# Performance work log

Measured on AMD Instinct MI355X. Metric: run time of the kernel, lower is better.

Reference implementation:

```python
import jax, jax.numpy as jnp
import numpy as np

GRID = (128, 128, 16)
VSIZE = 0.5  # voxel_size, pc_range = 0
B, V, N, K, C = 2, 100000, 8192, 8, 64
EPS = 1e-5
OFFSETS = [(dx, dy, dz) for dx in (-1, 0, 1) for dy in (-1, 0, 1) for dz in (-1, 0, 1)]


def setup_inputs() -> dict:
    key = jax.random.key(0)
    ks = jax.random.split(key, 8)
    world = jnp.array([GRID[0] * VSIZE, GRID[1] * VSIZE, GRID[2] * VSIZE], jnp.float32)
    keypoints = jax.random.uniform(ks[0], (B, N, K, 3), jnp.float32) * world
    query_feature = jax.random.normal(ks[1], (B, N, C), jnp.float32)
    voxel_feature = jax.random.normal(ks[2], (B, V, C), jnp.float32)
    # unique voxel coords per batch (hash-map / sparse-tensor semantics)
    cells = GRID[0] * GRID[1] * GRID[2]
    perm = jax.vmap(lambda k: jax.random.permutation(k, cells)[:V])(jax.random.split(ks[3], B))
    x = perm // (GRID[1] * GRID[2])
    rem = perm % (GRID[1] * GRID[2])
    voxel_coords = jnp.stack([x, rem // GRID[2], rem % GRID[2]], -1).astype(jnp.int32)
    W1 = jax.random.normal(ks[4], (27, C, C), jnp.float32) * 0.05
    W2 = jax.random.normal(ks[5], (27, C, C), jnp.float32) * 0.05
    proj_W = jax.random.normal(ks[6], (C, C), jnp.float32) / np.sqrt(C).astype(np.float32)
    proj_b = jnp.zeros((C,), jnp.float32)
    return dict(keypoints=keypoints, query_feature=query_feature,
                voxel_feature=voxel_feature, voxel_coords=voxel_coords,
                W1=W1, bn1_gamma=jnp.ones((C,), jnp.float32), bn1_beta=jnp.zeros((C,), jnp.float32),
                W2=W2, bn2_gamma=jnp.ones((C,), jnp.float32), bn2_beta=jnp.zeros((C,), jnp.float32),
                proj_W=proj_W, proj_b=proj_b)


def _subm_conv(feats, grid, cb, cxyz, W):
    # feats: (M, C); grid: (B, X, Y, Z) int32 flat row index or -1; W: (27, Cin, Cout)
    out = jnp.zeros((feats.shape[0], W.shape[-1]), feats.dtype)
    for k, (dx, dy, dz) in enumerate(OFFSETS):
        nx, ny, nz = cxyz[:, 0] + dx, cxyz[:, 1] + dy, cxyz[:, 2] + dz
        valid = (nx >= 0) & (nx < GRID[0]) & (ny >= 0) & (ny < GRID[1]) & (nz >= 0) & (nz < GRID[2])
        nidx = grid[cb, jnp.clip(nx, 0, GRID[0] - 1), jnp.clip(ny, 0, GRID[1] - 1), jnp.clip(nz, 0, GRID[2] - 1)]
        nidx = jnp.where(valid, nidx, -1)
        nf = jnp.where((nidx >= 0)[:, None], feats[jnp.maximum(nidx, 0)], jnp.zeros((), feats.dtype))
        out = out + nf @ W[k]
    return out


def _bn_relu(x, gamma, beta):
    # BatchNorm1d in training mode: batch stats (biased var), then ReLU
    mu = x.mean(0)
    var = jnp.var(x, axis=0)
    return jax.nn.relu((x - mu) * jax.lax.rsqrt(var + EPS) * gamma + beta)


def reference(keypoints, query_feature, voxel_feature, voxel_coords,
              W1, bn1_gamma, bn1_beta, W2, bn2_gamma, bn2_beta, proj_W, proj_b):
    coords = voxel_coords.reshape(-1, 3).astype(jnp.int32)
    cb = jnp.repeat(jnp.arange(B, dtype=jnp.int32), V)
    # dense grid hash: cell -> flat voxel row, -1 if empty (replaces Python dict)
    grid = jnp.full((B,) + GRID, -1, jnp.int32)
    grid = grid.at[cb, coords[:, 0], coords[:, 1], coords[:, 2]].set(jnp.arange(B * V, dtype=jnp.int32))
    feats = voxel_feature.reshape(-1, C)
    feats = _bn_relu(_subm_conv(feats, grid, cb, coords, W1), bn1_gamma, bn1_beta)
    feats = _bn_relu(_subm_conv(feats, grid, cb, coords, W2), bn2_gamma, bn2_beta)
    # quantize keypoints (pc_range = 0, trunc == floor since coords >= 0)
    q = (keypoints / VSIZE).astype(jnp.int32)
    q = jnp.clip(q, 0, jnp.array(GRID, jnp.int32) - 1)  # (B, N, K, 3)
    bidx = jnp.arange(B, dtype=jnp.int32)[:, None, None]
    idx = grid[bidx, q[..., 0], q[..., 1], q[..., 2]]   # (B, N, K); -1 -> fallback row 0
    sampled = feats[jnp.maximum(idx, 0)]                 # (B, N, K, C)
    fused = (sampled.mean(2) + query_feature) @ proj_W.T + proj_b
    voxel_indices = jnp.concatenate(
        [jnp.broadcast_to(bidx[..., None], (B, N, K, 1)), q], axis=-1).reshape(-1, 4)
    return fused, voxel_indices
```

## Files before the change

kernel.cpp:

```cpp
#include <hip/hip_runtime.h>
#include <hip/hip_bf16.h>
#include <math.h>

#define GX 128
#define GY 128
#define GZ 16
#define CELLS (GX*GY*GZ)
#define NCELLT (NB*CELLS)
#define NB 2
#define NV 100000
#define NM (NB*NV)
#define NN 8192
#define NK 8
#define NC 64
#define EPSV 1e-5f
#define TM 128
#define NTILE 196
#define NBLK (8*NTILE)

typedef __attribute__((ext_vector_type(8))) short short8;
typedef __attribute__((ext_vector_type(4))) float floatx4;

__device__ __forceinline__ float bf2f(unsigned short u) {
    unsigned int x = ((unsigned int)u) << 16;
    return __builtin_bit_cast(float, x);
}
__device__ __forceinline__ unsigned short f2bf(float f) {
    unsigned int u = __builtin_bit_cast(unsigned int, f);
    return (unsigned short)((u + 0x7fffu + ((u >> 16) & 1u)) >> 16);
}

__global__ void k_init(int* __restrict__ grid, float* __restrict__ stats,
                       unsigned short* __restrict__ featA) {
    int i = blockIdx.x * 256 + threadIdx.x;
    if (i < NCELLT) grid[i] = -1;
    else if (i < NCELLT + 512) stats[i - NCELLT] = 0.f;
    else if (i < NCELLT + 512 + 64) featA[(size_t)NM * 64 + (i - NCELLT - 512)] = 0;
}

__global__ void k_scatter(const int* __restrict__ coords, int* __restrict__ grid) {
    int gid = blockIdx.x * 256 + threadIdx.x;
    if (gid >= NM) return;
    int b = (gid >= NV) ? 1 : 0;
    int x = coords[gid * 3 + 0];
    int y = coords[gid * 3 + 1];
    int z = coords[gid * 3 + 2];
    grid[((b * GX + x) * GY + y) * GZ + z] = gid;
}

__global__ void k_count(const int* __restrict__ grid, int* __restrict__ bcnt) {
    __shared__ int wt[4];
    int t = threadIdx.x;
    int occ = (grid[blockIdx.x * 256 + t] >= 0) ? 1 : 0;
    int w = t >> 6;
    unsigned long long m = __ballot(occ);
    if ((t & 63) == 0) wt[w] = __popcll(m);
    __syncthreads();
    if (t == 0) bcnt[blockIdx.x] = wt[0] + wt[1] + wt[2] + wt[3];
}

__global__ void k_scan2048(const int* __restrict__ bcnt, int* __restrict__ boff) {
    __shared__ int s[256];
    int t = threadIdx.x;
    int v[8], sum = 0;
    #pragma unroll
    for (int j = 0; j < 8; ++j) {
        int x = bcnt[t * 8 + j];
        v[j] = sum;
        sum += x;
    }
    s[t] = sum;
    __syncthreads();
    for (int off = 1; off < 256; off <<= 1) {
        int x = (t >= off) ? s[t - off] : 0;
        __syncthreads();
        s[t] += x;
        __syncthreads();
    }
    int excl = s[t] - sum;
    #pragma unroll
    for (int j = 0; j < 8; ++j) boff[t * 8 + j] = excl + v[j];
}

__global__ void k_assign(const int* __restrict__ gold, const int* __restrict__ boff,
                         int* __restrict__ gnew, int* __restrict__ perm,
                         int* __restrict__ scell) {
    __shared__ int wt[4];
    int t = threadIdx.x;
    int cell = blockIdx.x * 256 + t;
    int old = gold[cell];
    int occ = (old >= 0) ? 1 : 0;
    int w = t >> 6, lane = t & 63;
    unsigned long long m = __ballot(occ);
    int lp = __popcll(m & ((1ULL << lane) - 1ULL));
    if (lane == 63) wt[w] = lp + occ;
    __syncthreads();
    int wbase = 0;
    #pragma unroll
    for (int j = 0; j < 4; ++j) if (j < w) wbase += wt[j];
    int nid = boff[blockIdx.x] + wbase + lp;
    if (occ) {
        gnew[cell] = nid;
        perm[nid] = old;
        scell[nid] = cell;
    } else {
        gnew[cell] = -1;
    }
}

__global__ void k_fb(const int* __restrict__ vcoords, const int* __restrict__ gnew,
                     int* __restrict__ fbp) {
    if (threadIdx.x == 0 && blockIdx.x == 0) {
        int cell = (vcoords[0] * GY + vcoords[1]) * GZ + vcoords[2];
        fbp[0] = gnew[cell];
    }
}

__global__ void k_wprep(const float* __restrict__ W1, const float* __restrict__ W2,
                        unsigned short* __restrict__ Wt1, unsigned short* __restrict__ Wt2) {
    int e = blockIdx.x * 256 + threadIdx.x;
    if (e >= 27 * 512) return;
    int lane = e & 63;
    int fr = (e >> 6) & 7;
    int k = e >> 9;
    int ct = fr >> 1, ks = fr & 1;
    int quad = lane >> 4, n16 = lane & 15;
    int co = ct * 16 + n16;
    #pragma unroll
    for (int j = 0; j < 8; ++j) {
        int ci = ks * 32 + quad * 8 + j;
        Wt1[(size_t)e * 8 + j] = f2bf(W1[(k << 12) + ci * 64 + co]);
        Wt2[(size_t)e * 8 + j] = f2bf(W2[(k << 12) + ci * 64 + co]);
    }
}

__global__ void k_tobf16s(const float* __restrict__ in, const int* __restrict__ perm,
                          unsigned short* __restrict__ out) {
    int i = blockIdx.x * 256 + threadIdx.x;
    if (i >= NM * 8) return;
    int mrow = i >> 3, part = i & 7;
    int src = perm[mrow];
    const float4* s = (const float4*)(in + (size_t)src * 64 + part * 8);
    float4 a = s[0], b = s[1];
    ushort4 lo, hi;
    lo.x = f2bf(a.x); lo.y = f2bf(a.y); lo.z = f2bf(a.z); lo.w = f2bf(a.w);
    hi.x = f2bf(b.x); hi.y = f2bf(b.y); hi.z = f2bf(b.z); hi.w = f2bf(b.w);
    ushort4* d = (ushort4*)(out + (size_t)mrow * 64 + part * 8);
    d[0] = lo; d[1] = hi;
}

__global__ __launch_bounds__(256, 4) void k_conv(
    const unsigned short* __restrict__ feats, const int* __restrict__ scell,
    const int* __restrict__ grid, const unsigned short* __restrict__ Wt,
    unsigned short* __restrict__ out, float* __restrict__ gsum, float* __restrict__ gsq)
{
    __shared__ int s_nidx[27 * TM];
    __shared__ int s_c[TM];

    int tid = threadIdx.x;
    int bid = blockIdx.x;
    int tile = (bid & 7) * NTILE + (bid >> 3);
    int m0 = tile * TM;

    if (tid < TM) {
        int m = m0 + tid;
        s_c[tid] = (m < NM) ? scell[m] : -1;
    }
    __syncthreads();

    for (int e = tid; e < 27 * TM; e += 256) {
        int k = e >> 7;
        int r = e & (TM - 1);
        int dx = k / 9 - 1, dy = (k / 3) % 3 - 1, dz = k % 3 - 1;
        int cell = s_c[r];
        int ni = -1;
        if (cell >= 0) {
            int x = (cell >> 11) & 127, y = (cell >> 4) & 127, z = cell & 15;
            int nx = x + dx, ny = y + dy, nz = z + dz;
            if (nx >= 0 && nx < GX && ny >= 0 && ny < GY && nz >= 0 && nz < GZ)
                ni = grid[cell + dx * (GY * GZ) + dy * GZ + dz];
        }
        s_nidx[k * TM + r] = ni;
    }
    __syncthreads();

    int w = tid >> 6, lane = tid & 63;
    int quad = lane >> 4, n16 = lane & 15;
    const int* nrow = s_nidx + w * 32 + n16;
    const unsigned short* fq = feats + quad * 8;

    short8 afr[2][4];
    short8 bfr[8];

    auto issueA = [&](int k, short8* af) {
        int ni0 = nrow[k * TM];
        int ni1 = nrow[k * TM + 16];
        ni0 = (ni0 < 0) ? NM : ni0;
        ni1 = (ni1 < 0) ? NM : ni1;
        const unsigned short* r0 = fq + (size_t)ni0 * 64;
        const unsigned short* r1 = fq + (size_t)ni1 * 64;
        af[0] = *(const short8*)(r0);
        af[1] = *(const short8*)(r0 + 32);
        af[2] = *(const short8*)(r1);
        af[3] = *(const short8*)(r1 + 32);
    };
    auto issueB = [&](int k, short8* bf) {
        const unsigned short* wb = Wt + ((size_t)k * 512 + lane) * 8;
        #pragma unroll
        for (int fr = 0; fr < 8; ++fr)
            bf[fr] = *(const short8*)(wb + fr * 512);
    };

    floatx4 acc[2][4];
    #pragma unroll
    for (int rt = 0; rt < 2; ++rt)
        #pragma unroll
        for (int ct = 0; ct < 4; ++ct)
            acc[rt][ct] = (floatx4){0.f, 0.f, 0.f, 0.f};

    issueA(0, afr[0]);
    __builtin_amdgcn_sched_barrier(0);

    #pragma unroll
    for (int k = 0; k < 27; ++k) {
        issueB(k, bfr);
        if (k + 1 < 27) issueA(k + 1, afr[(k + 1) & 1]);
        __builtin_amdgcn_sched_barrier(0);

        const short8* ac = afr[k & 1];
        #pragma unroll
        for (int ks = 0; ks < 2; ++ks)
            #pragma unroll
            for (int rt = 0; rt < 2; ++rt)
                #pragma unroll
                for (int ct = 0; ct < 4; ++ct)
                    acc[rt][ct] = __builtin_amdgcn_mfma_f32_16x16x32_bf16(
                        ac[rt * 2 + ks], bfr[ct * 2 + ks], acc[rt][ct], 0, 0, 0);
        __builtin_amdgcn_sched_barrier(0);
    }

    #pragma unroll
    for (int rt = 0; rt < 2; ++rt) {
        int rbase = m0 + w * 32 + rt * 16 + quad * 4;
        #pragma unroll
        for (int rg = 0; rg < 4; ++rg) {
            int m = rbase + rg;
            if (m < NM) {
                #pragma unroll
                for (int ct = 0; ct < 4; ++ct)
                    out[(size_t)m * 64 + ct * 16 + n16] = f2bf(acc[rt][ct][rg]);
            }
        }
    }

    float ps[4], pq[4];
    #pragma unroll
    for (int ct = 0; ct < 4; ++ct) { ps[ct] = 0.f; pq[ct] = 0.f; }
    #pragma unroll
    for (int rt = 0; rt < 2; ++rt)
        #pragma unroll
        for (int ct = 0; ct < 4; ++ct)
            #pragma unroll
            for (int rg = 0; rg < 4; ++rg) {
                float v = acc[rt][ct][rg];
                ps[ct] += v;
                pq[ct] += v * v;
            }
    #pragma unroll
    for (int ct = 0; ct < 4; ++ct) {
        ps[ct] += __shfl_xor(ps[ct], 16);
        ps[ct] += __shfl_xor(ps[ct], 32);
        pq[ct] += __shfl_xor(pq[ct], 16);
        pq[ct] += __shfl_xor(pq[ct], 32);
    }
    __syncthreads();
    float* red = (float*)s_nidx;
    if (lane < 16) {
        #pragma unroll
        for (int ct = 0; ct < 4; ++ct) {
            red[w * 64 + ct * 16 + n16]       = ps[ct];
            red[256 + w * 64 + ct * 16 + n16] = pq[ct];
        }
    }
    __syncthreads();
    if (tid < 64) {
        float ts = 0.f, tq = 0.f;
        #pragma unroll
        for (int ww = 0; ww < 4; ++ww) {
            ts += red[ww * 64 + tid];
            tq += red[256 + ww * 64 + tid];
        }
        atomicAdd(gsum + tid, ts);
        atomicAdd(gsq + tid, tq);
    }
}

__global__ void k_bncoef(const float* __restrict__ gsum, const float* __restrict__ gsq,
                         const float* __restrict__ gamma, const float* __restrict__ beta,
                         float* __restrict__ coef) {
    int c = threadIdx.x;
    if (c >= 64) return;
    float mu = gsum[c] / (float)NM;
    float var = gsq[c] / (float)NM - mu * mu;
    float scale = gamma[c] / sqrtf(var + EPSV);
    coef[c] = scale;
    coef[64 + c] = beta[c] - mu * scale;
}

__global__ void k_bnapply(const unsigned short* __restrict__ in, const float* __restrict__ coef,
                          unsigned short* __restrict__ out) {
    int i = blockIdx.x * 256 + threadIdx.x;
    if (i >= NM * 8) return;
    int c8 = (i & 7) * 8;
    uint4 v = ((const uint4*)in)[i];
    unsigned int vv[4] = {v.x, v.y, v.z, v.w};
    unsigned int oo[4];
    #pragma unroll
    for (int j = 0; j < 4; ++j) {
        int c = c8 + j * 2;
        float lo = bf2f((unsigned short)(vv[j] & 0xffffu));
        float hi = bf2f((unsigned short)(vv[j] >> 16));
        lo = fmaxf(lo * coef[c]     + coef[64 + c],     0.f);
        hi = fmaxf(hi * coef[c + 1] + coef[64 + c + 1], 0.f);
        oo[j] = (unsigned int)f2bf(lo) | ((unsigned int)f2bf(hi) << 16);
    }
    uint4 o = {oo[0], oo[1], oo[2], oo[3]};
    ((uint4*)out)[i] = o;
}

__global__ __launch_bounds__(256) void k_sample(
    const float* __restrict__ kp, const float* __restrict__ query,
    const unsigned short* __restrict__ conv2, const float* __restrict__ coef2,
    const int* __restrict__ grid, const int* __restrict__ fbp,
    const float* __restrict__ projW, const float* __restrict__ projB,
    float* __restrict__ out_fused, float* __restrict__ out_vi)
{
    __shared__ float s_pw[64 * 65];
    __shared__ float s_mean[4][64];
    __shared__ int   s_idx[4][8];

    int tid = threadIdx.x;
    for (int e = tid; e < 4096; e += 256) {
        int co = e >> 6, c = e & 63;
        s_pw[co * 65 + c] = projW[e];
    }

    int w = tid >> 6, lane = tid & 63;
    int row = blockIdx.x * 4 + w;
    int b = row >> 13;
    float sc = coef2[lane];
    float sh = coef2[64 + lane];
    int fb = fbp[0];
    __syncthreads();

    if (lane < 8) {
        int kk = lane;
        const float* kpp = kp + ((size_t)row * 8 + kk) * 3;
        int qx = min(max((int)(kpp[0] * 2.0f), 0), GX - 1);
        int qy = min(max((int)(kpp[1] * 2.0f), 0), GY - 1);
        int qz = min(max((int)(kpp[2] * 2.0f), 0), GZ - 1);
        s_idx[w][kk] = grid[((b * GX + qx) * GY + qy) * GZ + qz];
        float4 vi = make_float4((float)b, (float)qx, (float)qy, (float)qz);
        *(float4*)(out_vi + ((size_t)row * 8 + kk) * 4) = vi;
    }
    __syncthreads();

    float acc = 0.f;
    #pragma unroll
    for (int kk = 0; kk < 8; ++kk) {
        int gi = s_idx[w][kk];
        gi = gi < 0 ? fb : gi;
        float v = bf2f(conv2[(size_t)gi * 64 + lane]);
        acc += fmaxf(v * sc + sh, 0.f);
    }
    float mean = acc * 0.125f + query[(size_t)row * 64 + lane];
    s_mean[w][lane] = mean;
    __syncthreads();

    float f = projB[lane];
    const float* pwr = s_pw + lane * 65;
    const float* mv = s_mean[w];
    #pragma unroll 8
    for (int c = 0; c < 64; ++c) f += mv[c] * pwr[c];
    out_fused[(size_t)row * 64 + lane] = f;
}

extern "C" void kernel_launch(void* const* d_in, const int* in_sizes, int n_in,
                              void* d_out, int out_size, void* d_ws, size_t ws_size,
                              hipStream_t stream) {
    const float* keypoints = (const float*)d_in[0];
    const float* query     = (const float*)d_in[1];
    const float* vfeat     = (const float*)d_in[2];
    const int*   vcoords   = (const int*)d_in[3];
    const float* W1        = (const float*)d_in[4];
    const float* g1        = (const float*)d_in[5];
    const float* b1        = (const float*)d_in[6];
    const float* W2        = (const float*)d_in[7];
    const float* g2        = (const float*)d_in[8];
    const float* b2        = (const float*)d_in[9];
    const float* pW        = (const float*)d_in[10];
    const float* pb        = (const float*)d_in[11];

    char* ws = (char*)d_ws;
    int*            gold  = (int*)ws;
    int*            gnew  = (int*)(ws + 2097152);
    float*          stats = (float*)(ws + 4194304);
    int*            fbp   = (int*)(ws + 4196352);
    int*            bcnt  = (int*)(ws + 4196608);
    int*            boff  = (int*)(ws + 4204800);
    int*            perm  = (int*)(ws + 4212992);
    int*            scell = (int*)(ws + 5012992);
    unsigned short* Wt1   = (unsigned short*)(ws + 5812992);
    unsigned short* Wt2   = (unsigned short*)(ws + 6034176);
    unsigned short* featA = (unsigned short*)(ws + 6255360);
    unsigned short* convo = (unsigned short*)(ws + 31855488);

    float* sum1 = stats,       *sq1 = stats + 64,  *coef1 = stats + 128;
    float* sum2 = stats + 256, *sq2 = stats + 320, *coef2 = stats + 384;

    int initN = NCELLT + 512 + 64;
    k_init<<<(initN + 255) / 256, 256, 0, stream>>>(gold, stats, featA);
    k_scatter<<<(NM + 255) / 256, 256, 0, stream>>>(vcoords, gold);

    k_count<<<NCELLT / 256, 256, 0, stream>>>(gold, bcnt);
    k_scan2048<<<1, 256, 0, stream>>>(bcnt, boff);
    k_assign<<<NCELLT / 256, 256, 0, stream>>>(gold, boff, gnew, perm, scell);
    k_fb<<<1, 64, 0, stream>>>(vcoords, gnew, fbp);

    k_wprep<<<(27 * 512 + 255) / 256, 256, 0, stream>>>(W1, W2, Wt1, Wt2);
    k_tobf16s<<<(NM * 8 + 255) / 256, 256, 0, stream>>>(vfeat, perm, featA);

    k_conv<<<NBLK, 256, 0, stream>>>(featA, scell, gnew, Wt1, convo, sum1, sq1);
    k_bncoef<<<1, 64, 0, stream>>>(sum1, sq1, g1, b1, coef1);
    k_bnapply<<<(NM * 8 + 255) / 256, 256, 0, stream>>>(convo, coef1, featA);

    k_conv<<<NBLK, 256, 0, stream>>>(featA, scell, gnew, Wt2, convo, sum2, sq2);
    k_bncoef<<<1, 64, 0, stream>>>(sum2, sq2, g2, b2, coef2);

    float* out_fused = (float*)d_out;
    float* out_vi = out_fused + (size_t)NB * NN * NC;
    k_sample<<<(NB * NN) / 4, 256, 0, stream>>>(keypoints, query, convo, coef2, gnew, fbp,
                                                pW, pb, out_fused, out_vi);
}
```

Before: 378.5 us.

## Stage conv weight slices through double-buffered LDS instead of per-wave global loads

Each block now loads the 27 weight slices cooperatively into a double-buffered shared-memory array, with register staging for the next slice, instead of having each of the four waves load the full slice from global/L2. This cuts redundant weight traffic by four times per block. In exchange it adds a __syncthreads per offset and 16 KB of LDS, which may lower occupancy and serialize the waves.

```diff
diff --git a/kernel.cpp b/kernel.cpp
--- a/kernel.cpp
+++ b/kernel.cpp
@@ -156,6 +156,7 @@
 {
     __shared__ int s_nidx[27 * TM];
     __shared__ int s_c[TM];
+    __shared__ unsigned short s_bw[2][4096];
 
     int tid = threadIdx.x;
     int bid = blockIdx.x;
@@ -190,8 +191,18 @@
     const unsigned short* fq = feats + quad * 8;
 
     short8 afr[2][4];
-    short8 bfr[8];
-
+    uint4 sreg[2];
+
+    auto stageLoad = [&](int k) {
+        const uint4* src = (const uint4*)(Wt + (size_t)k * 4096) + tid;
+        sreg[0] = src[0];
+        sreg[1] = src[256];
+    };
+    auto stageStore = [&](int k) {
+        uint4* dst = (uint4*)s_bw[k & 1] + tid;
+        dst[0]   = sreg[0];
+        dst[256] = sreg[1];
+    };
     auto issueA = [&](int k, short8* af) {
         int ni0 = nrow[k * TM];
         int ni1 = nrow[k * TM + 16];
@@ -204,12 +215,6 @@
         af[2] = *(const short8*)(r1);
         af[3] = *(const short8*)(r1 + 32);
     };
-    auto issueB = [&](int k, short8* bf) {
-        const unsigned short* wb = Wt + ((size_t)k * 512 + lane) * 8;
-        #pragma unroll
-        for (int fr = 0; fr < 8; ++fr)
-            bf[fr] = *(const short8*)(wb + fr * 512);
-    };
 
     floatx4 acc[2][4];
     #pragma unroll
@@ -218,25 +223,37 @@
         for (int ct = 0; ct < 4; ++ct)
             acc[rt][ct] = (floatx4){0.f, 0.f, 0.f, 0.f};
 
+    stageLoad(0);
     issueA(0, afr[0]);
-    __builtin_amdgcn_sched_barrier(0);
+    stageStore(0);
+    __syncthreads();
 
     #pragma unroll
     for (int k = 0; k < 27; ++k) {
-        issueB(k, bfr);
-        if (k + 1 < 27) issueA(k + 1, afr[(k + 1) & 1]);
+        if (k + 1 < 27) {
+            stageLoad(k + 1);
+            issueA(k + 1, afr[(k + 1) & 1]);
+        }
         __builtin_amdgcn_sched_barrier(0);
 
-        const short8* ac = afr[k & 1];
-        #pragma unroll
-        for (int ks = 0; ks < 2; ++ks)
+        const unsigned short* bb = s_bw[k & 1];
+        #pragma unroll
+        for (int ks = 0; ks < 2; ++ks) {
+            short8 bfr[4];
+            #pragma unroll
+            for (int ct = 0; ct < 4; ++ct)
+                bfr[ct] = *(const short8*)(bb + (ct * 2 + ks) * 512 + lane * 8);
             #pragma unroll
             for (int rt = 0; rt < 2; ++rt)
                 #pragma unroll
                 for (int ct = 0; ct < 4; ++ct)
                     acc[rt][ct] = __builtin_amdgcn_mfma_f32_16x16x32_bf16(
-                        ac[rt * 2 + ks], bfr[ct * 2 + ks], acc[rt][ct], 0, 0, 0);
+                        afr[k & 1][rt * 2 + ks], bfr[ct], acc[rt][ct], 0, 0, 0);
+        }
         __builtin_amdgcn_sched_barrier(0);
+
+        if (k + 1 < 27) stageStore(k + 1);
+        __syncthreads();
     }
 
     #pragma unroll
```

Measured after the change: 439.7 us. +16.2%, slower.

## Double conv tile rows and stage weights in LDS in phases

Applied to the files above, without the earlier changes.

The sparse conv kernel now processes 256 rows per block (64 per wave) instead of 128. Weights for 7 kernel offsets at a time are staged in shared memory rather than loaded from global memory per wave. Neighbor indices are also computed per phase, and the weights are padded to 28 offsets with zeros so the four phases divide evenly. This is meant to cut redundant weight traffic and amortize it over more MFMAs, at the cost of higher register and LDS use (occupancy bound lowered to 2), a wasted zero offset, and extra barriers per phase.

```diff
diff --git a/kernel.cpp b/kernel.cpp
--- a/kernel.cpp
+++ b/kernel.cpp
@@ -14,9 +14,10 @@
 #define NK 8
 #define NC 64
 #define EPSV 1e-5f
-#define TM 128
-#define NTILE 196
+#define TM 256
+#define NTILE 98
 #define NBLK (8*NTILE)
+#define KPH 7
 
 typedef __attribute__((ext_vector_type(8))) short short8;
 typedef __attribute__((ext_vector_type(4))) float floatx4;
@@ -119,7 +120,7 @@
 __global__ void k_wprep(const float* __restrict__ W1, const float* __restrict__ W2,
                         unsigned short* __restrict__ Wt1, unsigned short* __restrict__ Wt2) {
     int e = blockIdx.x * 256 + threadIdx.x;
-    if (e >= 27 * 512) return;
+    if (e >= 28 * 512) return;
     int lane = e & 63;
     int fr = (e >> 6) & 7;
     int k = e >> 9;
@@ -129,8 +130,13 @@
     #pragma unroll
     for (int j = 0; j < 8; ++j) {
         int ci = ks * 32 + quad * 8 + j;
-        Wt1[(size_t)e * 8 + j] = f2bf(W1[(k << 12) + ci * 64 + co]);
-        Wt2[(size_t)e * 8 + j] = f2bf(W2[(k << 12) + ci * 64 + co]);
+        unsigned short w1 = 0, w2 = 0;
+        if (k < 27) {
+            w1 = f2bf(W1[(k << 12) + ci * 64 + co]);
+            w2 = f2bf(W2[(k << 12) + ci * 64 + co]);
+        }
+        Wt1[(size_t)e * 8 + j] = w1;
+        Wt2[(size_t)e * 8 + j] = w2;
     }
 }
 
@@ -149,12 +155,13 @@
     d[0] = lo; d[1] = hi;
 }
 
-__global__ __launch_bounds__(256, 4) void k_conv(
+__global__ __launch_bounds__(256, 2) void k_conv(
     const unsigned short* __restrict__ feats, const int* __restrict__ scell,
     const int* __restrict__ grid, const unsigned short* __restrict__ Wt,
     unsigned short* __restrict__ out, float* __restrict__ gsum, float* __restrict__ gsq)
 {
-    __shared__ int s_nidx[27 * TM];
+    __shared__ unsigned short s_b[KPH * 4096];
+    __shared__ int s_nidx[KPH * TM];
     __shared__ int s_c[TM];
 
     int tid = threadIdx.x;
@@ -162,86 +169,94 @@
     int tile = (bid & 7) * NTILE + (bid >> 3);
     int m0 = tile * TM;
 
-    if (tid < TM) {
+    {
         int m = m0 + tid;
         s_c[tid] = (m < NM) ? scell[m] : -1;
     }
-    __syncthreads();
-
-    for (int e = tid; e < 27 * TM; e += 256) {
-        int k = e >> 7;
-        int r = e & (TM - 1);
-        int dx = k / 9 - 1, dy = (k / 3) % 3 - 1, dz = k % 3 - 1;
-        int cell = s_c[r];
-        int ni = -1;
-        if (cell >= 0) {
-            int x = (cell >> 11) & 127, y = (cell >> 4) & 127, z = cell & 15;
-            int nx = x + dx, ny = y + dy, nz = z + dz;
-            if (nx >= 0 && nx < GX && ny >= 0 && ny < GY && nz >= 0 && nz < GZ)
-                ni = grid[cell + dx * (GY * GZ) + dy * GZ + dz];
-        }
-        s_nidx[k * TM + r] = ni;
-    }
-    __syncthreads();
 
     int w = tid >> 6, lane = tid & 63;
     int quad = lane >> 4, n16 = lane & 15;
-    const int* nrow = s_nidx + w * 32 + n16;
     const unsigned short* fq = feats + quad * 8;
 
-    short8 afr[2][4];
-    short8 bfr[8];
-
-    auto issueA = [&](int k, short8* af) {
-        int ni0 = nrow[k * TM];
-        int ni1 = nrow[k * TM + 16];
-        ni0 = (ni0 < 0) ? NM : ni0;
-        ni1 = (ni1 < 0) ? NM : ni1;
-        const unsigned short* r0 = fq + (size_t)ni0 * 64;
-        const unsigned short* r1 = fq + (size_t)ni1 * 64;
-        af[0] = *(const short8*)(r0);
-        af[1] = *(const short8*)(r0 + 32);
-        af[2] = *(const short8*)(r1);
-        af[3] = *(const short8*)(r1 + 32);
+    short8 afr[2][8];
+
+    auto issueA = [&](int kk, short8* af) {
+        #pragma unroll
+        for (int rt = 0; rt < 4; ++rt) {
+            int ni = s_nidx[kk * TM + w * 64 + rt * 16 + n16];
+            ni = (ni < 0) ? NM : ni;
+            const unsigned short* r0 = fq + (size_t)ni * 64;
+            af[rt * 2 + 0] = *(const short8*)(r0);
+            af[rt * 2 + 1] = *(const short8*)(r0 + 32);
+        }
     };
-    auto issueB = [&](int k, short8* bf) {
-        const unsigned short* wb = Wt + ((size_t)k * 512 + lane) * 8;
-        #pragma unroll
-        for (int fr = 0; fr < 8; ++fr)
-            bf[fr] = *(const short8*)(wb + fr * 512);
-    };
-
-    floatx4 acc[2][4];
-    #pragma unroll
-    for (int rt = 0; rt < 2; ++rt)
+
+    floatx4 acc[4][4];
+    #pragma unroll
+    for (int rt = 0; rt < 4; ++rt)
         #pragma unroll
         for (int ct = 0; ct < 4; ++ct)
             acc[rt][ct] = (floatx4){0.f, 0.f, 0.f, 0.f};
 
-    issueA(0, afr[0]);
-    __builtin_amdgcn_sched_barrier(0);
-
-    #pragma unroll
-    for (int k = 0; k < 27; ++k) {
-        issueB(k, bfr);
-        if (k + 1 < 27) issueA(k + 1, afr[(k + 1) & 1]);
+    const uint4* wt4 = (const uint4*)Wt;
+
+    for (int ph = 0; ph < 4; ++ph) {
+        int k0 = ph * KPH;
+        __syncthreads();
+        #pragma unroll
+        for (int i = 0; i < KPH * 2; ++i)
+            ((uint4*)s_b)[i * 256 + tid] = wt4[(size_t)k0 * 512 + i * 256 + tid];
+        #pragma unroll
+        for (int j = 0; j < KPH; ++j) {
+            int e = j * 256 + tid;
+            int kk = e >> 8;
+            int r = e & 255;
+            int k = k0 + kk;
+            int ni = -1;
+            if (k < 27) {
+                int dx = k / 9 - 1, dy = (k / 3) % 3 - 1, dz = k % 3 - 1;
+                int cell = s_c[r];
+                if (cell >= 0) {
+                    int x = (cell >> 11) & 127, y = (cell >> 4) & 127, z = cell & 15;
+                    int nx = x + dx, ny = y + dy, nz = z + dz;
+                    if (nx >= 0 && nx < GX && ny >= 0 && ny < GY && nz >= 0 && nz < GZ)
+                        ni = grid[cell + dx * (GY * GZ) + dy * GZ + dz];
+                }
+            }
+            s_nidx[kk * TM + r] = ni;
+        }
+        __syncthreads();
+
+        issueA(0, afr[0]);
         __builtin_amdgcn_sched_barrier(0);
 
-        const short8* ac = afr[k & 1];
-        #pragma unroll
-        for (int ks = 0; ks < 2; ++ks)
+        #pragma unroll
+        for (int kk = 0; kk < KPH; ++kk) {
+            if (kk + 1 < KPH) issueA(kk + 1, afr[(kk + 1) & 1]);
+            __builtin_amdgcn_sched_barrier(0);
+
+            const unsigned short* bb = s_b + kk * 4096;
+            short8 bfr[8];
             #pragma unroll
-            for (int rt = 0; rt < 2; ++rt)
+            for (int fr = 0; fr < 8; ++fr)
+                bfr[fr] = *(const short8*)(bb + fr * 512 + lane * 8);
+
+            const short8* ac = afr[kk & 1];
+            #pragma unroll
+            for (int ks = 0; ks < 2; ++ks)
                 #pragma unroll
-                for (int ct = 0; ct < 4; ++ct)
-                    acc[rt][ct] = __builtin_amdgcn_mfma_f32_16x16x32_bf16(
-                        ac[rt * 2 + ks], bfr[ct * 2 + ks], acc[rt][ct], 0, 0, 0);
-        __builtin_amdgcn_sched_barrier(0);
-    }
-
-    #pragma unroll
-    for (int rt = 0; rt < 2; ++rt) {
-        int rbase = m0 + w * 32 + rt * 16 + quad * 4;
+                for (int rt = 0; rt < 4; ++rt)
+                    #pragma unroll
+                    for (int ct = 0; ct < 4; ++ct)
+                        acc[rt][ct] = __builtin_amdgcn_mfma_f32_16x16x32_bf16(
+                            ac[rt * 2 + ks], bfr[ct * 2 + ks], acc[rt][ct], 0, 0, 0);
+            __builtin_amdgcn_sched_barrier(0);
+        }
+    }
+
+    #pragma unroll
+    for (int rt = 0; rt < 4; ++rt) {
+        int rbase = m0 + w * 64 + rt * 16 + quad * 4;
         #pragma unroll
         for (int rg = 0; rg < 4; ++rg) {
             int m = rbase + rg;
@@ -257,7 +272,7 @@
     #pragma unroll
     for (int ct = 0; ct < 4; ++ct) { ps[ct] = 0.f; pq[ct] = 0.f; }
     #pragma unroll
-    for (int rt = 0; rt < 2; ++rt)
+    for (int rt = 0; rt < 4; ++rt)
         #pragma unroll
         for (int ct = 0; ct < 4; ++ct)
             #pragma unroll
@@ -411,9 +426,9 @@
     int*            perm  = (int*)(ws + 4212992);
     int*            scell = (int*)(ws + 5012992);
     unsigned short* Wt1   = (unsigned short*)(ws + 5812992);
-    unsigned short* Wt2   = (unsigned short*)(ws + 6034176);
-    unsigned short* featA = (unsigned short*)(ws + 6255360);
-    unsigned short* convo = (unsigned short*)(ws + 31855488);
+    unsigned short* Wt2   = (unsigned short*)(ws + 6042368);
+    unsigned short* featA = (unsigned short*)(ws + 6271744);
+    unsigned short* convo = (unsigned short*)(ws + 31871872);
 
     float* sum1 = stats,       *sq1 = stats + 64,  *coef1 = stats + 128;
     float* sum2 = stats + 256, *sq2 = stats + 320, *coef2 = stats + 384;
@@ -427,7 +442,7 @@
     k_assign<<<NCELLT / 256, 256, 0, stream>>>(gold, boff, gnew, perm, scell);
     k_fb<<<1, 64, 0, stream>>>(vcoords, gnew, fbp);
 
-    k_wprep<<<(27 * 512 + 255) / 256, 256, 0, stream>>>(W1, W2, Wt1, Wt2);
+    k_wprep<<<(28 * 512 + 255) / 256, 256, 0, stream>>>(W1, W2, Wt1, Wt2);
     k_tobf16s<<<(NM * 8 + 255) / 256, 256, 0, stream>>>(vfeat, perm, featA);
 
     k_conv<<<NBLK, 256, 0, stream>>>(featA, scell, gnew, Wt1, convo, sum1, sq1);
```

Measured after the change: 342.6 us. -9.5%, faster.
